# Kernel tuning notes

Measured on AMD Instinct MI355X. Metric: run time of the kernel, lower is better.

The kernel has to match this reference:

```python
import jax, jax.numpy as jnp
import numpy as np

N_NODES = 100000
N_EDGES = 3200000
N_GRAPHS = 1000
IN_DIM = 10
HID = 20
N_CLASSES = 2
BN_EPS = 1e-5


def setup_inputs() -> dict:
    key = jax.random.key(0)
    ks = jax.random.split(key, 12)
    x = jax.random.normal(ks[0], (N_NODES, IN_DIM), dtype=jnp.float32)
    edge_index = jax.random.randint(ks[1], (2, N_EDGES), 0, N_NODES, dtype=jnp.int64)
    batch = jnp.sort(jax.random.randint(ks[2], (N_NODES,), 0, N_GRAPHS, dtype=jnp.int64))
    def lin(k, fan_in, fan_out):
        bound = 1.0 / np.sqrt(fan_in)
        kw, kb = jax.random.split(k)
        W = jax.random.uniform(kw, (fan_in, fan_out), jnp.float32, -bound, bound)
        b = jax.random.uniform(kb, (fan_out,), jnp.float32, -bound, bound)
        return W, b
    W1, b1 = lin(ks[3], IN_DIM, HID)
    W2, b2 = lin(ks[4], HID, HID)
    W3, b3 = lin(ks[5], HID, HID)
    fcW, fcb = lin(ks[6], HID, N_CLASSES)
    ones = jnp.ones((HID,), jnp.float32)
    zeros = jnp.zeros((HID,), jnp.float32)
    return {
        "x": x, "edge_index": edge_index, "batch": batch,
        "W1": W1, "b1": b1, "g1": ones, "beta1": zeros,
        "W2": W2, "b2": b2, "g2": ones, "beta2": zeros,
        "W3": W3, "b3": b3, "g3": ones, "beta3": zeros,
        "fcW": fcW, "fcb": fcb,
    }


def _gin_layer(h, src, dst, W, b, g, beta):
    # GIN aggregation: (1+eps)*x_i + sum_{j->i} x_j, eps = 0
    agg = jax.ops.segment_sum(h[src], dst, num_segments=N_NODES)  # [N, d]
    h = (h + agg) @ W + b                                          # MLP (single Linear)
    mu = jnp.mean(h, axis=0)                                       # BatchNorm (batch stats)
    var = jnp.mean(jnp.square(h - mu), axis=0)
    h = (h - mu) * jax.lax.rsqrt(var + BN_EPS) * g + beta
    return jax.nn.relu(h)                                          # dropout p=0 is identity


def reference(x, edge_index, batch, W1, b1, g1, beta1, W2, b2, g2, beta2,
              W3, b3, g3, beta3, fcW, fcb):
    src, dst = edge_index[0], edge_index[1]
    h = _gin_layer(x, src, dst, W1, b1, g1, beta1)
    h = _gin_layer(h, src, dst, W2, b2, g2, beta2)
    h = _gin_layer(h, src, dst, W3, b3, g3, beta3)
    graph_emb = jax.ops.segment_sum(h, batch, num_segments=N_GRAPHS)  # global add pool
    return graph_emb @ fcW + fcb
```

## Files before the change

### kernel.cpp

```cpp
#include <hip/hip_runtime.h>
#include <hip/hip_bf16.h>
#include <hip/hip_fp16.h>

#define N_NODES  100000
#define N_EDGES  3200000
#define N_GRAPHS 1000
#define IN_DIM   10
#define HID      20
#define BN_EPS   1e-5f

#define BSH   8
#define NB    ((N_NODES + 255) / 256)
#define CAP   9216
#define FB    512
#define FCHUNK ((N_EDGES + FB - 1) / FB)
#define NBG   ((N_NODES + 31) / 32)
#define HS    24

__global__ __launch_bounds__(512) void fill_direct(const int* __restrict__ src,
                                                   const int* __restrict__ dst,
                                                   int* __restrict__ bcur,
                                                   unsigned* __restrict__ packed) {
    __shared__ int cnt[NB];
    __shared__ int base[NB];
    int t = threadIdx.x;
    for (int i = t; i < NB; i += 512) cnt[i] = 0;
    __syncthreads();
    int e0 = blockIdx.x * FCHUNK;
    int e1 = min(e0 + FCHUNK, N_EDGES);
    for (int e = e0 + t; e < e1; e += 512)
        atomicAdd(&cnt[dst[e] >> BSH], 1);
    __syncthreads();
    for (int i = t; i < NB; i += 512) {
        int c = cnt[i];
        base[i] = c ? atomicAdd(&bcur[i], c) : 0;
        cnt[i] = 0;
    }
    __syncthreads();
    for (int e = e0 + t; e < e1; e += 512) {
        int d = dst[e];
        int b = d >> BSH;
        int r = atomicAdd(&cnt[b], 1);
        packed[(size_t)b * CAP + base[b] + r] =
            (unsigned)src[e] | ((unsigned)(d & 255) << 24);
    }
}

__global__ void scan_buckets(const int* __restrict__ bcur, int* __restrict__ off) {
    __shared__ int lds[512];
    int t = threadIdx.x;
    int v = (t < NB) ? bcur[t] : 0;
    int val = v;
    lds[t] = val; __syncthreads();
    for (int o = 1; o < 512; o <<= 1) {
        int a = (t >= o) ? lds[t - o] : 0;
        __syncthreads();
        val += a; lds[t] = val;
        __syncthreads();
    }
    if (t < NB) off[t] = val - v;
    if (t == 0) off[NB] = N_EDGES;
}

__global__ __launch_bounds__(512) void sort_bucket(const unsigned* __restrict__ packed,
                                                   const int* __restrict__ bcnt,
                                                   const int* __restrict__ off,
                                                   int* __restrict__ csr,
                                                   int* __restrict__ rp) {
    __shared__ unsigned ebuf[CAP];
    __shared__ int cnt[256];
    __shared__ int cur[256];
    int b = blockIdx.x, t = threadIdx.x;
    int m = bcnt[b];
    int o = off[b];
    const unsigned* pb = packed + (size_t)b * CAP;
    for (int i = t; i < m; i += 512) ebuf[i] = pb[i];
    if (t < 256) cnt[t] = 0;
    __syncthreads();
    for (int i = t; i < m; i += 512) atomicAdd(&cnt[ebuf[i] >> 24], 1);
    __syncthreads();
    int v = 0, val = 0;
    if (t < 256) { v = cnt[t]; val = v; cur[t] = val; }
    __syncthreads();
    for (int ofs = 1; ofs < 256; ofs <<= 1) {
        int add = (t < 256 && t >= ofs) ? cur[t - ofs] : 0;
        __syncthreads();
        if (t < 256) { val += add; cur[t] = val; }
        __syncthreads();
    }
    if (t < 256) {
        int node = b * 256 + t;
        if (node <= N_NODES) rp[node] = o + (val - v);
        cur[t] = val - v;
    }
    __syncthreads();
    for (int i = t; i < m; i += 512) {
        unsigned p = ebuf[i];
        int l = p >> 24;
        int pos = atomicAdd(&cur[l], 1);
        csr[o + pos] = (int)(p & 0xFFFFFFu);
    }
}

template<int DIN, bool BN>
__global__ __launch_bounds__(256) void gather_mlp8(
        const float* __restrict__ hf,
        const __half* __restrict__ hh,
        const int* __restrict__ rp, const int* __restrict__ csr,
        const float* __restrict__ W,
        const float* __restrict__ bias,
        const float* __restrict__ ssin,
        __half* __restrict__ hout,
        float* __restrict__ partials)
{
    __shared__ float sW[DIN * HID];
    __shared__ float sb[HID];
    __shared__ float sss[2 * HID];
    __shared__ float red[4][2 * HID];
    __shared__ __half sh_h[32][HS];
    int t = threadIdx.x;
    for (int i = t; i < DIN * HID; i += 256) sW[i] = W[i];
    if (t < HID) sb[t] = bias[t];
    if constexpr (BN) { if (t < 2 * HID) sss[t] = ssin[t]; }
    __syncthreads();

    int node = blockIdx.x * 32 + (t >> 3);
    int sub  = t & 7;
    float u[DIN];
#pragma unroll
    for (int k = 0; k < DIN; k++) u[k] = 0.0f;

    auto accw = [&](const unsigned* w) {
#pragma unroll
        for (int q = 0; q < 10; q++) {
            float2 f = __half22float2(*(const __half2*)&w[q]);
            float v0 = f.x, v1 = f.y;
            if constexpr (BN) {
                v0 = fmaxf(fmaf(v0, sss[2*q+0], sss[HID+2*q+0]), 0.f);
                v1 = fmaxf(fmaf(v1, sss[2*q+1], sss[HID+2*q+1]), 0.f);
            }
            u[2*q] += v0; u[2*q+1] += v1;
        }
    };

    if (node < N_NODES) {
        int e0 = rp[node], e1 = rp[node + 1];
        if constexpr (DIN == 20) {
            if (sub == 0) {
                const __half* r = hh + (size_t)node * HS;
                unsigned w[10];
                uint4 A = *(const uint4*)r;
                uint4 B = *(const uint4*)(r + 8);
                uint2 C = *(const uint2*)(r + 16);
                w[0]=A.x; w[1]=A.y; w[2]=A.z; w[3]=A.w;
                w[4]=B.x; w[5]=B.y; w[6]=B.z; w[7]=B.w;
                w[8]=C.x; w[9]=C.y;
                accw(w);
            }
            int e = e0 + sub;
            for (; e + 8 < e1; e += 16) {
                int s0 = csr[e], s1 = csr[e + 8];
                const __half* r0 = hh + (size_t)s0 * HS;
                const __half* r1 = hh + (size_t)s1 * HS;
                uint4 A0 = *(const uint4*)r0;
                uint4 B0 = *(const uint4*)(r0 + 8);
                uint2 C0 = *(const uint2*)(r0 + 16);
                uint4 A1 = *(const uint4*)r1;
                uint4 B1 = *(const uint4*)(r1 + 8);
                uint2 C1 = *(const uint2*)(r1 + 16);
                unsigned w0[10] = {A0.x,A0.y,A0.z,A0.w,B0.x,B0.y,B0.z,B0.w,C0.x,C0.y};
                unsigned w1[10] = {A1.x,A1.y,A1.z,A1.w,B1.x,B1.y,B1.z,B1.w,C1.x,C1.y};
                accw(w0); accw(w1);
            }
            if (e < e1) {
                const __half* r0 = hh + (size_t)csr[e] * HS;
                uint4 A = *(const uint4*)r0;
                uint4 B = *(const uint4*)(r0 + 8);
                uint2 C = *(const uint2*)(r0 + 16);
                unsigned w[10] = {A.x,A.y,A.z,A.w,B.x,B.y,B.z,B.w,C.x,C.y};
                accw(w);
            }
        } else {
            if (sub == 0) {
                const float2* hv = (const float2*)(hf + (size_t)node * DIN);
#pragma unroll
                for (int q = 0; q < 5; q++) {
                    float2 a = hv[q];
                    u[2*q] += a.x; u[2*q+1] += a.y;
                }
            }
            int e = e0 + sub;
            for (; e + 8 < e1; e += 16) {
                int s0 = csr[e], s1 = csr[e + 8];
                const float2* a0 = (const float2*)(hf + (size_t)s0 * DIN);
                const float2* a1 = (const float2*)(hf + (size_t)s1 * DIN);
                float2 r0[5], r1[5];
#pragma unroll
                for (int q = 0; q < 5; q++) r0[q] = a0[q];
#pragma unroll
                for (int q = 0; q < 5; q++) r1[q] = a1[q];
#pragma unroll
                for (int q = 0; q < 5; q++) {
                    u[2*q]   += r0[q].x + r1[q].x;
                    u[2*q+1] += r0[q].y + r1[q].y;
                }
            }
            if (e < e1) {
                const float2* a0 = (const float2*)(hf + (size_t)csr[e] * DIN);
#pragma unroll
                for (int q = 0; q < 5; q++) {
                    float2 x0 = a0[q];
                    u[2*q] += x0.x; u[2*q+1] += x0.y;
                }
            }
        }
    }

#pragma unroll
    for (int k = 0; k < DIN; k++) {
        u[k] += __shfl_xor(u[k], 1);
        u[k] += __shfl_xor(u[k], 2);
        u[k] += __shfl_xor(u[k], 4);
    }

    const int c0 = (sub & 3) * 5;
    float out[5];
#pragma unroll
    for (int j = 0; j < 5; j++) out[j] = sb[c0 + j];
#pragma unroll
    for (int k = 0; k < DIN; k++) {
        float uk = u[k];
#pragma unroll
        for (int j = 0; j < 5; j++)
            out[j] = fmaf(uk, sW[k * HID + c0 + j], out[j]);
    }
    bool live = (node < N_NODES) && (sub < 4);
    if (live) {
        int nl = t >> 3;
#pragma unroll
        for (int j = 0; j < 5; j++) sh_h[nl][c0 + j] = __float2half(out[j]);
    }

    float msk = live ? 1.0f : 0.0f;
    float s1[5], s2[5];
#pragma unroll
    for (int j = 0; j < 5; j++) {
        float o = out[j] * msk;
        s1[j] = o; s2[j] = o * out[j];
    }
    for (int o = 8; o < 64; o <<= 1) {
#pragma unroll
        for (int j = 0; j < 5; j++) {
            s1[j] += __shfl_down(s1[j], o);
            s2[j] += __shfl_down(s2[j], o);
        }
    }
    int lane = t & 63, wave = t >> 6;
    if (lane < 4) {
#pragma unroll
        for (int j = 0; j < 5; j++) {
            red[wave][lane * 5 + j]       = s1[j];
            red[wave][HID + lane * 5 + j] = s2[j];
        }
    }
    __syncthreads();
    if (t < 32) {
        int n2 = blockIdx.x * 32 + t;
        if (n2 < N_NODES) {
            const uint4* sp = (const uint4*)&sh_h[t][0];
            uint4 a0 = sp[0], a1 = sp[1];
            uint2 a2 = ((const uint2*)sp)[4];
            uint4* gp = (uint4*)(hout + (size_t)n2 * HS);
            gp[0] = a0; gp[1] = a1;
            ((uint2*)gp)[4] = a2;
        }
    }
    if (t < 2 * HID)
        partials[(size_t)t * NBG + blockIdx.x] =
            red[0][t] + red[1][t] + red[2][t] + red[3][t];
}

__global__ __launch_bounds__(256) void bn_prep(const float* __restrict__ partials,
                                               const float* __restrict__ g,
                                               const float* __restrict__ beta,
                                               float* __restrict__ ss) {
    int c = blockIdx.x, t = threadIdx.x;
    double a1 = 0.0, a2 = 0.0;
    for (int i = t; i < NBG; i += 256) {
        a1 += (double)partials[(size_t)c * NBG + i];
        a2 += (double)partials[(size_t)(c + HID) * NBG + i];
    }
    for (int o = 32; o; o >>= 1) {
        a1 += __shfl_down(a1, o);
        a2 += __shfl_down(a2, o);
    }
    __shared__ double r1[4], r2[4];
    int lane = t & 63, wave = t >> 6;
    if (lane == 0) { r1[wave] = a1; r2[wave] = a2; }
    __syncthreads();
    if (t == 0) {
        double su = r1[0] + r1[1] + r1[2] + r1[3];
        double sq = r2[0] + r2[1] + r2[2] + r2[3];
        double mu  = su / (double)N_NODES;
        double var = sq / (double)N_NODES - mu * mu;
        float sc = g[c] * (float)(1.0 / sqrt(var + (double)BN_EPS));
        ss[c]       = sc;
        ss[HID + c] = beta[c] - (float)mu * sc;
    }
}

__global__ void gptr_kernel(const int* __restrict__ batch, int* __restrict__ gptr) {
    int n = blockIdx.x * blockDim.x + threadIdx.x;
    if (n >= N_NODES) return;
    int g = batch[n];
    int gp = (n == 0) ? -1 : batch[n - 1];
    for (int q = gp + 1; q <= g; q++) gptr[q] = n;
    if (n == N_NODES - 1)
        for (int q = g + 1; q <= N_GRAPHS; q++) gptr[q] = N_NODES;
}

__global__ __launch_bounds__(256) void pool_fc(const __half* __restrict__ h,
                                               const int* __restrict__ gptr,
                                               const float* __restrict__ ss,
                                               const float* __restrict__ fcW,
                                               const float* __restrict__ fcb,
                                               float* __restrict__ out) {
    __shared__ float red[12][HID];
    __shared__ float sss[2 * HID];
    __shared__ float pl[HID];
    int g = blockIdx.x, t = threadIdx.x;
    if (t < 2 * HID) sss[t] = ss[t];
    __syncthreads();
    int n0 = gptr[g], n1 = gptr[g + 1];
    if (t < 240) {
        int c = t % HID, grp = t / HID;
        float s = 0.0f;
        for (int n = n0 + grp; n < n1; n += 12) {
            float v = fmaf(__half2float(h[(size_t)n * HS + c]), sss[c], sss[HID + c]);
            s += v > 0.0f ? v : 0.0f;
        }
        red[grp][c] = s;
    }
    __syncthreads();
    if (t < HID) {
        float a = 0.0f;
#pragma unroll
        for (int q = 0; q < 12; q++) a += red[q][t];
        pl[t] = a;
    }
    __syncthreads();
    if (t < 2) {
        float o = fcb[t];
#pragma unroll
        for (int k = 0; k < HID; k++) o = fmaf(pl[k], fcW[k * 2 + t], o);
        out[g * 2 + t] = o;
    }
}

extern "C" void kernel_launch(void* const* d_in, const int* in_sizes, int n_in,
                              void* d_out, int out_size, void* d_ws, size_t ws_size,
                              hipStream_t stream) {
    const float* x     = (const float*)d_in[0];
    const int*   eidx  = (const int*)d_in[1];
    const int*   batch = (const int*)d_in[2];
    const float* W1 = (const float*)d_in[3];
    const float* b1 = (const float*)d_in[4];
    const float* g1 = (const float*)d_in[5];
    const float* be1 = (const float*)d_in[6];
    const float* W2 = (const float*)d_in[7];
    const float* b2 = (const float*)d_in[8];
    const float* g2 = (const float*)d_in[9];
    const float* be2 = (const float*)d_in[10];
    const float* W3 = (const float*)d_in[11];
    const float* b3 = (const float*)d_in[12];
    const float* g3 = (const float*)d_in[13];
    const float* be3 = (const float*)d_in[14];
    const float* fcW = (const float*)d_in[15];
    const float* fcb = (const float*)d_in[16];
    float* out = (float*)d_out;

    const int* src = eidx;
    const int* dst = eidx + N_EDGES;

    char* ws = (char*)d_ws;
    __half* hA16   = (__half*)(ws + 0);
    __half* hB16   = (__half*)(ws + 4800000);
    unsigned* packed = (unsigned*)(ws + 0);
    int*   csr     = (int*)(ws + 16000000);
    int*   rp      = (int*)(ws + 28800000);
    int*   off     = (int*)(ws + 29200128);
    int*   bcur    = (int*)(ws + 29203328);
    float* partials= (float*)(ws + 29209728);
    float* ss1     = (float*)(ws + 29709728);
    float* ss2     = (float*)(ws + 29709888);
    float* ss3     = (float*)(ws + 29710048);
    int*   gptr    = (int*)(ws + 29710208);

    const int BLK = 256;

    hipMemsetAsync(bcur, 0, NB * sizeof(int), stream);
    fill_direct<<<FB, 512, 0, stream>>>(src, dst, bcur, packed);
    scan_buckets<<<1, 512, 0, stream>>>(bcur, off);
    sort_bucket<<<NB, 512, 0, stream>>>(packed, bcur, off, csr, rp);
    gptr_kernel<<<(N_NODES + BLK - 1) / BLK, BLK, 0, stream>>>(batch, gptr);

    gather_mlp8<IN_DIM, false><<<NBG, BLK, 0, stream>>>(x, (const __half*)nullptr,
        rp, csr, W1, b1, ss1, hA16, partials);
    bn_prep<<<HID, BLK, 0, stream>>>(partials, g1, be1, ss1);

    gather_mlp8<HID, true><<<NBG, BLK, 0, stream>>>((const float*)nullptr, hA16,
        rp, csr, W2, b2, ss1, hB16, partials);
    bn_prep<<<HID, BLK, 0, stream>>>(partials, g2, be2, ss2);

    gather_mlp8<HID, true><<<NBG, BLK, 0, stream>>>((const float*)nullptr, hB16,
        rp, csr, W3, b3, ss2, hA16, partials);
    bn_prep<<<HID, BLK, 0, stream>>>(partials, g3, be3, ss3);

    pool_fc<<<N_GRAPHS, BLK, 0, stream>>>(hA16, gptr, ss3, fcW, fcb, out);
}
```

Baseline: 317.1 us.

## Split node features into aligned lo/hi arrays and stage dst in LDS

Node feature rows are split into a 32-byte aligned low part (16 halves or 8 floats) and a separate small high part, so each gathered row takes one aligned 32B line plus a small side read, instead of a 48B padded row spanning lines. A split_x kernel reformats x into this layout before layer 1. fill_direct now uses half as many blocks and caches each chunk's dst values in shared memory, avoiding a second global read of dst. The costs are an extra kernel launch, a second memory stream per gather, and lower parallelism in fill_direct.

```diff
diff --git a/kernel.cpp b/kernel.cpp
--- a/kernel.cpp
+++ b/kernel.cpp
@@ -12,15 +12,15 @@
 #define BSH   8
 #define NB    ((N_NODES + 255) / 256)
 #define CAP   9216
-#define FB    512
+#define FB    256
 #define FCHUNK ((N_EDGES + FB - 1) / FB)
 #define NBG   ((N_NODES + 31) / 32)
-#define HS    24
 
 __global__ __launch_bounds__(512) void fill_direct(const int* __restrict__ src,
                                                    const int* __restrict__ dst,
                                                    int* __restrict__ bcur,
                                                    unsigned* __restrict__ packed) {
+    __shared__ int sdst[FCHUNK];
     __shared__ int cnt[NB];
     __shared__ int base[NB];
     int t = threadIdx.x;
@@ -28,8 +28,12 @@
     __syncthreads();
     int e0 = blockIdx.x * FCHUNK;
     int e1 = min(e0 + FCHUNK, N_EDGES);
-    for (int e = e0 + t; e < e1; e += 512)
-        atomicAdd(&cnt[dst[e] >> BSH], 1);
+    int m = e1 - e0;
+    for (int i = t; i < m; i += 512) {
+        int d = dst[e0 + i];
+        sdst[i] = d;
+        atomicAdd(&cnt[d >> BSH], 1);
+    }
     __syncthreads();
     for (int i = t; i < NB; i += 512) {
         int c = cnt[i];
@@ -37,12 +41,12 @@
         cnt[i] = 0;
     }
     __syncthreads();
-    for (int e = e0 + t; e < e1; e += 512) {
-        int d = dst[e];
+    for (int i = t; i < m; i += 512) {
+        int d = sdst[i];
         int b = d >> BSH;
         int r = atomicAdd(&cnt[b], 1);
         packed[(size_t)b * CAP + base[b] + r] =
-            (unsigned)src[e] | ((unsigned)(d & 255) << 24);
+            (unsigned)src[e0 + i] | ((unsigned)(d & 255) << 24);
     }
 }
 
@@ -102,22 +106,36 @@
     }
 }
 
+__global__ void split_x(const float* __restrict__ x,
+                        float* __restrict__ xlo, float* __restrict__ xhi) {
+    int n = blockIdx.x * blockDim.x + threadIdx.x;
+    if (n >= N_NODES) return;
+    const float2* xp = (const float2*)(x + (size_t)n * 10);
+    float2 v0 = xp[0], v1 = xp[1], v2 = xp[2], v3 = xp[3], v4 = xp[4];
+    float4* lp = (float4*)(xlo + (size_t)n * 8);
+    float4 a; a.x = v0.x; a.y = v0.y; a.z = v1.x; a.w = v1.y;
+    float4 b; b.x = v2.x; b.y = v2.y; b.z = v3.x; b.w = v3.y;
+    lp[0] = a; lp[1] = b;
+    *(float2*)(xhi + (size_t)n * 2) = v4;
+}
+
 template<int DIN, bool BN>
 __global__ __launch_bounds__(256) void gather_mlp8(
-        const float* __restrict__ hf,
-        const __half* __restrict__ hh,
+        const float* __restrict__ flo, const float* __restrict__ fhi,
+        const __half* __restrict__ hlo, const __half* __restrict__ hhi,
         const int* __restrict__ rp, const int* __restrict__ csr,
         const float* __restrict__ W,
         const float* __restrict__ bias,
         const float* __restrict__ ssin,
-        __half* __restrict__ hout,
+        __half* __restrict__ olo,
+        __half* __restrict__ ohi,
         float* __restrict__ partials)
 {
     __shared__ float sW[DIN * HID];
     __shared__ float sb[HID];
     __shared__ float sss[2 * HID];
     __shared__ float red[4][2 * HID];
-    __shared__ __half sh_h[32][HS];
+    __shared__ __half sh[32][24];
     int t = threadIdx.x;
     for (int i = t; i < DIN * HID; i += 256) sW[i] = W[i];
     if (t < HID) sb[t] = bias[t];
@@ -130,88 +148,76 @@
 #pragma unroll
     for (int k = 0; k < DIN; k++) u[k] = 0.0f;
 
-    auto accw = [&](const unsigned* w) {
-#pragma unroll
-        for (int q = 0; q < 10; q++) {
-            float2 f = __half22float2(*(const __half2*)&w[q]);
-            float v0 = f.x, v1 = f.y;
-            if constexpr (BN) {
-                v0 = fmaxf(fmaf(v0, sss[2*q+0], sss[HID+2*q+0]), 0.f);
-                v1 = fmaxf(fmaf(v1, sss[2*q+1], sss[HID+2*q+1]), 0.f);
-            }
-            u[2*q] += v0; u[2*q+1] += v1;
-        }
+    auto acch2 = [&](unsigned w, int q) {
+        __half2 h2 = *(const __half2*)&w;
+        float2 f = __half22float2(h2);
+        float v0 = f.x, v1 = f.y;
+        if constexpr (BN) {
+            v0 = fmaxf(fmaf(v0, sss[2*q+0], sss[HID+2*q+0]), 0.f);
+            v1 = fmaxf(fmaf(v1, sss[2*q+1], sss[HID+2*q+1]), 0.f);
+        }
+        u[2*q] += v0; u[2*q+1] += v1;
+    };
+    auto accrow20 = [&](uint4 A, uint4 B, uint2 C) {
+        acch2(A.x, 0); acch2(A.y, 1); acch2(A.z, 2); acch2(A.w, 3);
+        acch2(B.x, 4); acch2(B.y, 5); acch2(B.z, 6); acch2(B.w, 7);
+        acch2(C.x, 8); acch2(C.y, 9);
     };
 
     if (node < N_NODES) {
         int e0 = rp[node], e1 = rp[node + 1];
         if constexpr (DIN == 20) {
             if (sub == 0) {
-                const __half* r = hh + (size_t)node * HS;
-                unsigned w[10];
-                uint4 A = *(const uint4*)r;
-                uint4 B = *(const uint4*)(r + 8);
-                uint2 C = *(const uint2*)(r + 16);
-                w[0]=A.x; w[1]=A.y; w[2]=A.z; w[3]=A.w;
-                w[4]=B.x; w[5]=B.y; w[6]=B.z; w[7]=B.w;
-                w[8]=C.x; w[9]=C.y;
-                accw(w);
+                const uint4* l = (const uint4*)(hlo + (size_t)node * 16);
+                uint4 A = l[0], B = l[1];
+                uint2 C = *(const uint2*)(hhi + (size_t)node * 4);
+                accrow20(A, B, C);
             }
             int e = e0 + sub;
             for (; e + 8 < e1; e += 16) {
                 int s0 = csr[e], s1 = csr[e + 8];
-                const __half* r0 = hh + (size_t)s0 * HS;
-                const __half* r1 = hh + (size_t)s1 * HS;
-                uint4 A0 = *(const uint4*)r0;
-                uint4 B0 = *(const uint4*)(r0 + 8);
-                uint2 C0 = *(const uint2*)(r0 + 16);
-                uint4 A1 = *(const uint4*)r1;
-                uint4 B1 = *(const uint4*)(r1 + 8);
-                uint2 C1 = *(const uint2*)(r1 + 16);
-                unsigned w0[10] = {A0.x,A0.y,A0.z,A0.w,B0.x,B0.y,B0.z,B0.w,C0.x,C0.y};
-                unsigned w1[10] = {A1.x,A1.y,A1.z,A1.w,B1.x,B1.y,B1.z,B1.w,C1.x,C1.y};
-                accw(w0); accw(w1);
+                const uint4* l0 = (const uint4*)(hlo + (size_t)s0 * 16);
+                const uint4* l1 = (const uint4*)(hlo + (size_t)s1 * 16);
+                uint4 A0 = l0[0], B0 = l0[1];
+                uint2 C0 = *(const uint2*)(hhi + (size_t)s0 * 4);
+                uint4 A1 = l1[0], B1 = l1[1];
+                uint2 C1 = *(const uint2*)(hhi + (size_t)s1 * 4);
+                accrow20(A0, B0, C0);
+                accrow20(A1, B1, C1);
             }
             if (e < e1) {
-                const __half* r0 = hh + (size_t)csr[e] * HS;
-                uint4 A = *(const uint4*)r0;
-                uint4 B = *(const uint4*)(r0 + 8);
-                uint2 C = *(const uint2*)(r0 + 16);
-                unsigned w[10] = {A.x,A.y,A.z,A.w,B.x,B.y,B.z,B.w,C.x,C.y};
-                accw(w);
+                int s0 = csr[e];
+                const uint4* l0 = (const uint4*)(hlo + (size_t)s0 * 16);
+                uint4 A = l0[0], B = l0[1];
+                uint2 C = *(const uint2*)(hhi + (size_t)s0 * 4);
+                accrow20(A, B, C);
             }
         } else {
+            auto accrow10 = [&](float4 A, float4 B, float2 C) {
+                u[0] += A.x; u[1] += A.y; u[2] += A.z; u[3] += A.w;
+                u[4] += B.x; u[5] += B.y; u[6] += B.z; u[7] += B.w;
+                u[8] += C.x; u[9] += C.y;
+            };
             if (sub == 0) {
-                const float2* hv = (const float2*)(hf + (size_t)node * DIN);
-#pragma unroll
-                for (int q = 0; q < 5; q++) {
-                    float2 a = hv[q];
-                    u[2*q] += a.x; u[2*q+1] += a.y;
-                }
+                const float4* l = (const float4*)(flo + (size_t)node * 8);
+                accrow10(l[0], l[1], *(const float2*)(fhi + (size_t)node * 2));
             }
             int e = e0 + sub;
             for (; e + 8 < e1; e += 16) {
                 int s0 = csr[e], s1 = csr[e + 8];
-                const float2* a0 = (const float2*)(hf + (size_t)s0 * DIN);
-                const float2* a1 = (const float2*)(hf + (size_t)s1 * DIN);
-                float2 r0[5], r1[5];
-#pragma unroll
-                for (int q = 0; q < 5; q++) r0[q] = a0[q];
-#pragma unroll
-                for (int q = 0; q < 5; q++) r1[q] = a1[q];
-#pragma unroll
-                for (int q = 0; q < 5; q++) {
-                    u[2*q]   += r0[q].x + r1[q].x;
-                    u[2*q+1] += r0[q].y + r1[q].y;
-                }
+                const float4* l0 = (const float4*)(flo + (size_t)s0 * 8);
+                const float4* l1 = (const float4*)(flo + (size_t)s1 * 8);
+                float4 A0 = l0[0], B0 = l0[1];
+                float2 C0 = *(const float2*)(fhi + (size_t)s0 * 2);
+                float4 A1 = l1[0], B1 = l1[1];
+                float2 C1 = *(const float2*)(fhi + (size_t)s1 * 2);
+                accrow10(A0, B0, C0);
+                accrow10(A1, B1, C1);
             }
             if (e < e1) {
-                const float2* a0 = (const float2*)(hf + (size_t)csr[e] * DIN);
-#pragma unroll
-                for (int q = 0; q < 5; q++) {
-                    float2 x0 = a0[q];
-                    u[2*q] += x0.x; u[2*q+1] += x0.y;
-                }
+                int s0 = csr[e];
+                const float4* l0 = (const float4*)(flo + (size_t)s0 * 8);
+                accrow10(l0[0], l0[1], *(const float2*)(fhi + (size_t)s0 * 2));
             }
         }
     }
@@ -238,7 +244,7 @@
     if (live) {
         int nl = t >> 3;
 #pragma unroll
-        for (int j = 0; j < 5; j++) sh_h[nl][c0 + j] = __float2half(out[j]);
+        for (int j = 0; j < 5; j++) sh[nl][c0 + j] = __float2half(out[j]);
     }
 
     float msk = live ? 1.0f : 0.0f;
@@ -267,12 +273,12 @@
     if (t < 32) {
         int n2 = blockIdx.x * 32 + t;
         if (n2 < N_NODES) {
-            const uint4* sp = (const uint4*)&sh_h[t][0];
+            const uint4* sp = (const uint4*)&sh[t][0];
             uint4 a0 = sp[0], a1 = sp[1];
-            uint2 a2 = ((const uint2*)sp)[4];
-            uint4* gp = (uint4*)(hout + (size_t)n2 * HS);
-            gp[0] = a0; gp[1] = a1;
-            ((uint2*)gp)[4] = a2;
+            uint2 a2 = *(const uint2*)&sh[t][16];
+            uint4* lp = (uint4*)(olo + (size_t)n2 * 16);
+            lp[0] = a0; lp[1] = a1;
+            *(uint2*)(ohi + (size_t)n2 * 4) = a2;
         }
     }
     if (t < 2 * HID)
@@ -319,7 +325,8 @@
         for (int q = g + 1; q <= N_GRAPHS; q++) gptr[q] = N_NODES;
 }
 
-__global__ __launch_bounds__(256) void pool_fc(const __half* __restrict__ h,
+__global__ __launch_bounds__(256) void pool_fc(const __half* __restrict__ hlo,
+                                               const __half* __restrict__ hhi,
                                                const int* __restrict__ gptr,
                                                const float* __restrict__ ss,
                                                const float* __restrict__ fcW,
@@ -336,7 +343,9 @@
         int c = t % HID, grp = t / HID;
         float s = 0.0f;
         for (int n = n0 + grp; n < n1; n += 12) {
-            float v = fmaf(__half2float(h[(size_t)n * HS + c]), sss[c], sss[HID + c]);
+            float raw = (c < 16) ? __half2float(hlo[(size_t)n * 16 + c])
+                                 : __half2float(hhi[(size_t)n * 4 + (c - 16)]);
+            float v = fmaf(raw, sss[c], sss[HID + c]);
             s += v > 0.0f ? v : 0.0f;
         }
         red[grp][c] = s;
@@ -383,8 +392,12 @@
     const int* dst = eidx + N_EDGES;
 
     char* ws = (char*)d_ws;
-    __half* hA16   = (__half*)(ws + 0);
-    __half* hB16   = (__half*)(ws + 4800000);
+    __half* hAlo   = (__half*)(ws + 0);
+    __half* hAhi   = (__half*)(ws + 3200000);
+    __half* hBlo   = (__half*)(ws + 4000000);
+    __half* hBhi   = (__half*)(ws + 7200000);
+    float*  xlo    = (float*)(ws + 8000000);
+    float*  xhi    = (float*)(ws + 11200000);
     unsigned* packed = (unsigned*)(ws + 0);
     int*   csr     = (int*)(ws + 16000000);
     int*   rp      = (int*)(ws + 28800000);
@@ -403,18 +416,22 @@
     scan_buckets<<<1, 512, 0, stream>>>(bcur, off);
     sort_bucket<<<NB, 512, 0, stream>>>(packed, bcur, off, csr, rp);
     gptr_kernel<<<(N_NODES + BLK - 1) / BLK, BLK, 0, stream>>>(batch, gptr);
-
-    gather_mlp8<IN_DIM, false><<<NBG, BLK, 0, stream>>>(x, (const __half*)nullptr,
-        rp, csr, W1, b1, ss1, hA16, partials);
+    split_x<<<(N_NODES + BLK - 1) / BLK, BLK, 0, stream>>>(x, xlo, xhi);
+
+    gather_mlp8<IN_DIM, false><<<NBG, BLK, 0, stream>>>(xlo, xhi,
+        (const __half*)nullptr, (const __half*)nullptr,
+        rp, csr, W1, b1, ss1, hAlo, hAhi, partials);
     bn_prep<<<HID, BLK, 0, stream>>>(partials, g1, be1, ss1);
 
-    gather_mlp8<HID, true><<<NBG, BLK, 0, stream>>>((const float*)nullptr, hA16,
-        rp, csr, W2, b2, ss1, hB16, partials);
+    gather_mlp8<HID, true><<<NBG, BLK, 0, stream>>>((const float*)nullptr,
+        (const float*)nullptr, hAlo, hAhi,
+        rp, csr, W2, b2, ss1, hBlo, hBhi, partials);
     bn_prep<<<HID, BLK, 0, stream>>>(partials, g2, be2, ss2);
 
-    gather_mlp8<HID, true><<<NBG, BLK, 0, stream>>>((const float*)nullptr, hB16,
-        rp, csr, W3, b3, ss2, hA16, partials);
+    gather_mlp8<HID, true><<<NBG, BLK, 0, stream>>>((const float*)nullptr,
+        (const float*)nullptr, hBlo, hBhi,
+        rp, csr, W3, b3, ss2, hAlo, hAhi, partials);
     bn_prep<<<HID, BLK, 0, stream>>>(partials, g3, be3, ss3);
 
-    pool_fc<<<N_GRAPHS, BLK, 0, stream>>>(hA16, gptr, ss3, fcW, fcb, out);
-}
+    pool_fc<<<N_GRAPHS, BLK, 0, stream>>>(hAlo, hAhi, gptr, ss3, fcW, fcb, out);
+}
```

New measurement: 326.4 us. 2.9% more time.
